# Kernel tuning notes

Hardware: AMD Instinct MI355X
Metric: run time of the kernel (lower is better)

Reference implementation:

```python
import jax, jax.numpy as jnp
import numpy as np

HEADS = 16
DIM_HEAD = 64
RMS_EPS = 1.1920929e-07  # torch.finfo(float32).eps (torch RMSNorm eps=None default)
ROPE_THETA = 10000.0


def _rope(x):
    # x: [b, h, n, d]; rotary-embedding-torch style interleaved rotation
    n, d = x.shape[-2], x.shape[-1]
    inv_freq = 1.0 / (ROPE_THETA ** (jnp.arange(0, d, 2, dtype=jnp.float32) / d))
    t = jnp.arange(n, dtype=jnp.float32)
    freqs = t[:, None] * inv_freq[None, :]              # [n, d/2]
    cos = jnp.repeat(jnp.cos(freqs), 2, axis=-1)        # [n, d] interleaved
    sin = jnp.repeat(jnp.sin(freqs), 2, axis=-1)
    x1 = x[..., ::2]
    x2 = x[..., 1::2]
    rot = jnp.stack((-x2, x1), axis=-1).reshape(x.shape)  # rotate_half, interleaved pairs
    return x * cos + rot * sin


def setup_inputs() -> dict:
    key = jax.random.key(0)
    ks = jax.random.split(key, 6)
    b, n, dim = 2, 2048, 1024
    tokens = jax.random.normal(ks[0], (b, n, dim), dtype=jnp.float32)
    norm_weight = jnp.ones((dim,), dtype=jnp.float32)
    wq = jax.random.normal(ks[1], (dim, dim), dtype=jnp.float32) * 0.02
    wk = jax.random.normal(ks[2], (dim, dim), dtype=jnp.float32) * 0.02
    wv = jax.random.normal(ks[3], (dim, dim), dtype=jnp.float32) * 0.02
    wo = jax.random.normal(ks[4], (dim, dim), dtype=jnp.float32) * 0.02
    return {"tokens": tokens, "norm_weight": norm_weight, "wq": wq, "wk": wk, "wv": wv, "wo": wo}


def reference(tokens, norm_weight, wq, wk, wv, wo):
    b, n, dim = tokens.shape
    # RMSNorm (elementwise affine)
    x = tokens * jax.lax.rsqrt(jnp.mean(tokens * tokens, axis=-1, keepdims=True) + RMS_EPS)
    x = x * norm_weight
    # QKV projections (torch Linear: x @ W.T), split heads: b n (h d) -> b h n d
    def split(y):
        return y.reshape(b, n, HEADS, DIM_HEAD).transpose(0, 2, 1, 3)
    q = split(x @ wq.T) * (DIM_HEAD ** -0.5)
    k = split(x @ wk.T)
    v = split(x @ wv.T)
    # rotary embedding (no kv cache -> same positions for q and k)
    q = _rope(q)
    k = _rope(k)
    sim = jnp.einsum('bhid,bhjd->bhij', q, k)
    causal = jnp.triu(jnp.ones((n, n), dtype=bool), k=1)
    sim = jnp.where(causal, -jnp.finfo(sim.dtype).max, sim)
    attn = jax.nn.softmax(sim, axis=-1)
    out = jnp.einsum('bhij,bhjd->bhid', attn, v)
    out = out.transpose(0, 2, 1, 3).reshape(b, n, dim)  # merge heads
    return out @ wo.T
```

## Files before the change

kernel.cpp:

```cpp
#include <hip/hip_runtime.h>

typedef __bf16 bf16x8 __attribute__((ext_vector_type(8)));
typedef float f32x4 __attribute__((ext_vector_type(4)));

#define DIM 1024
#define NSEQ 2048

#define GL2LDS(g, l) __builtin_amdgcn_global_load_lds( \
    (const __attribute__((address_space(1))) void*)(g), \
    (__attribute__((address_space(3))) void*)(l), 16, 0, 0)

#define MFMA16(a, b, c) __builtin_amdgcn_mfma_f32_16x16x32_bf16(a, b, c, 0, 0, 0)

__global__ __launch_bounds__(256) void cvt_kernel(const float* __restrict__ s,
                                                  __bf16* __restrict__ d) {
    int i = (blockIdx.x * 256 + threadIdx.x) * 4;
    float4 f = *(const float4*)(s + i);
    union { uint2 u; __bf16 h[4]; } p;
    p.h[0] = (__bf16)f.x; p.h[1] = (__bf16)f.y;
    p.h[2] = (__bf16)f.z; p.h[3] = (__bf16)f.w;
    *(uint2*)(d + i) = p.u;
}

__global__ __launch_bounds__(256) void pre_kernel(const float* __restrict__ wq,
                                                  const float* __restrict__ wk,
                                                  const float* __restrict__ wv,
                                                  __bf16* __restrict__ dq,
                                                  __bf16* __restrict__ dk,
                                                  __bf16* __restrict__ dv,
                                                  float2* __restrict__ tbl,
                                                  int* __restrict__ counters,
                                                  const float* __restrict__ x,
                                                  const float* __restrict__ g,
                                                  __bf16* __restrict__ xo) {
    int bid = blockIdx.x;
    int t = threadIdx.x;
    if (bid == 0 && t < 8) counters[t] = 0;
    if (bid < 3072) {
        int slice = bid >> 10;
        const float* s = slice == 0 ? wq : (slice == 1 ? wk : wv);
        __bf16*      d = slice == 0 ? dq : (slice == 1 ? dk : dv);
        int i = ((bid & 1023) * 256 + t) * 4;
        float4 f = *(const float4*)(s + i);
        union { uint2 u; __bf16 h[4]; } p;
        p.h[0] = (__bf16)f.x; p.h[1] = (__bf16)f.y;
        p.h[2] = (__bf16)f.z; p.h[3] = (__bf16)f.w;
        *(uint2*)(d + i) = p.u;
    } else if (bid < 3328) {
        int e = (bid - 3072) * 256 + t;
        int pos = e >> 5, dp = e & 31;
        float inv = __expf(-(float)dp * (9.210340371976184f / 32.0f));
        float sn, cs;
        sincosf((float)pos * inv, &sn, &cs);
        tbl[e] = make_float2(cs, sn);
    } else {
        int row = bid - 3328;
        float4 xv = ((const float4*)(x + (size_t)row * DIM))[t];
        float ss = xv.x*xv.x + xv.y*xv.y + xv.z*xv.z + xv.w*xv.w;
        #pragma unroll
        for (int off = 32; off; off >>= 1) ss += __shfl_xor(ss, off, 64);
        __shared__ float red[4];
        if ((t & 63) == 0) red[t >> 6] = ss;
        __syncthreads();
        ss = red[0] + red[1] + red[2] + red[3];
        float r = rsqrtf(ss * (1.0f / 1024.0f) + 1.1920929e-07f);
        float4 gv = ((const float4*)g)[t];
        union { uint2 u; __bf16 h[4]; } p;
        p.h[0] = (__bf16)(xv.x * r * gv.x);
        p.h[1] = (__bf16)(xv.y * r * gv.y);
        p.h[2] = (__bf16)(xv.z * r * gv.z);
        p.h[3] = (__bf16)(xv.w * r * gv.w);
        *(uint2*)(xo + (size_t)row * DIM + t * 4) = p.u;
    }
}

template <typename CT, bool ROPE>
__device__ __forceinline__ void gemm_body(const __bf16* __restrict__ A,
                                          const __bf16* __restrict__ B,
                                          CT* __restrict__ C,
                                          int mb, int nb, int ldc, float scale,
                                          __bf16* As, __bf16* Bs,
                                          const float2* __restrict__ tbl) {
    int t = threadIdx.x;
    int w = t >> 6, l = t & 63;
    int wm = (w >> 1) * 64, wn = (w & 1) * 64;
    int lrow = l & 15, lq = l >> 4;
    int sw = lrow & 7;
    f32x4 acc[4][4] = {};

    int srow = w * 32 + (l >> 3);
    int sc8 = ((l & 7) ^ ((l >> 3) & 7)) * 8;
    const __bf16* gA = A + (size_t)(mb * 128 + srow) * 1024 + sc8;
    const __bf16* gB = B + (size_t)(nb * 128 + srow) * 1024 + sc8;
    __bf16* lA = As + (size_t)(w * 32) * 64;
    __bf16* lB = Bs + (size_t)(w * 32) * 64;

    for (int kt = 0; kt < 16; ++kt) {
        int k0 = kt * 64;
        #pragma unroll
        for (int c = 0; c < 4; ++c) {
            GL2LDS(gA + (size_t)c * 8 * 1024 + k0, lA + c * 8 * 64);
            GL2LDS(gB + (size_t)c * 8 * 1024 + k0, lB + c * 8 * 64);
        }
        __syncthreads();
        #pragma unroll
        for (int ch = 0; ch < 2; ++ch) {
            bf16x8 af[4], bfr[4];
            #pragma unroll
            for (int i = 0; i < 4; ++i)
                af[i] = *(const bf16x8*)&As[(wm + i * 16 + lrow) * 64 + ((ch * 4 + lq) ^ sw) * 8];
            #pragma unroll
            for (int i = 0; i < 4; ++i)
                bfr[i] = *(const bf16x8*)&Bs[(wn + i * 16 + lrow) * 64 + ((ch * 4 + lq) ^ sw) * 8];
            #pragma unroll
            for (int rt = 0; rt < 4; ++rt)
                #pragma unroll
                for (int ct = 0; ct < 4; ++ct)
                    acc[rt][ct] = MFMA16(af[rt], bfr[ct], acc[rt][ct]);
        }
        __syncthreads();
    }
    #pragma unroll
    for (int rt = 0; rt < 4; ++rt)
        #pragma unroll
        for (int ct = 0; ct < 4; ++ct) {
            int colg = nb * 128 + wn + ct * 16 + lrow;
            int dp = ((ct * 16 + lrow) & 63) >> 1;
            #pragma unroll
            for (int r = 0; r < 4; ++r) {
                int rowg = mb * 128 + wm + rt * 16 + lq * 4 + r;
                float v = acc[rt][ct][r] * scale;
                if constexpr (ROPE) {
                    float p = __shfl_xor(v, 1, 64);
                    float2 cs = tbl[((rowg & (NSEQ - 1)) << 5) + dp];
                    v = (lrow & 1) ? (v * cs.x + p * cs.y)
                                   : (v * cs.x - p * cs.y);
                }
                C[(size_t)rowg * ldc + colg] = (CT)v;
            }
        }
}

__global__ __launch_bounds__(256) void qkv_kernel(const __bf16* __restrict__ x,
                                                  const __bf16* __restrict__ wq,
                                                  const __bf16* __restrict__ wk,
                                                  const __bf16* __restrict__ wv,
                                                  __bf16* __restrict__ qb,
                                                  __bf16* __restrict__ kb,
                                                  __bf16* __restrict__ vtb,
                                                  const float2* __restrict__ tbl) {
    __shared__ __bf16 As[128 * 64];
    __shared__ __bf16 Bs[128 * 64];
    int bm = blockIdx.x, bn = blockIdx.y, z = blockIdx.z;
    if (z == 0)      gemm_body<__bf16, true >(x,  wq, qb,  bm, bn, 1024,
                                       0.125f * 1.44269504088896340736f, As, Bs, tbl);
    else if (z == 1) gemm_body<__bf16, true >(x,  wk, kb,  bm, bn, 1024, 1.0f, As, Bs, tbl);
    else             gemm_body<__bf16, false>(wv, x,  vtb, bn, bm, 4096, 1.0f, As, Bs, tbl);
}

__global__ __launch_bounds__(256) void wo_kernel(const __bf16* __restrict__ A,
                                                 const __bf16* __restrict__ B,
                                                 float* __restrict__ C) {
    __shared__ __bf16 As[128 * 64];
    __shared__ __bf16 Bs[64 * 64];
    int mb = blockIdx.x, nb = blockIdx.y;
    int t = threadIdx.x;
    int w = t >> 6, l = t & 63;
    int wm = (w >> 1) * 64, wn = (w & 1) * 32;
    int lrow = l & 15, lq = l >> 4;
    int sw = lrow & 7;
    f32x4 acc[4][2] = {};

    int srowA = w * 32 + (l >> 3);
    int srowB = w * 16 + (l >> 3);
    int sc8 = ((l & 7) ^ ((l >> 3) & 7)) * 8;
    const __bf16* gA = A + (size_t)(mb * 128 + srowA) * 1024 + sc8;
    const __bf16* gB = B + (size_t)(nb * 64 + srowB) * 1024 + sc8;
    __bf16* lA = As + (size_t)(w * 32) * 64;
    __bf16* lB = Bs + (size_t)(w * 16) * 64;

    for (int kt = 0; kt < 16; ++kt) {
        int k0 = kt * 64;
        #pragma unroll
        for (int c = 0; c < 4; ++c)
            GL2LDS(gA + (size_t)c * 8 * 1024 + k0, lA + c * 8 * 64);
        #pragma unroll
        for (int c = 0; c < 2; ++c)
            GL2LDS(gB + (size_t)c * 8 * 1024 + k0, lB + c * 8 * 64);
        __syncthreads();
        #pragma unroll
        for (int ch = 0; ch < 2; ++ch) {
            bf16x8 af[4], bfr[2];
            #pragma unroll
            for (int i = 0; i < 4; ++i)
                af[i] = *(const bf16x8*)&As[(wm + i * 16 + lrow) * 64 + ((ch * 4 + lq) ^ sw) * 8];
            #pragma unroll
            for (int i = 0; i < 2; ++i)
                bfr[i] = *(const bf16x8*)&Bs[(wn + i * 16 + lrow) * 64 + ((ch * 4 + lq) ^ sw) * 8];
            #pragma unroll
            for (int rt = 0; rt < 4; ++rt)
                #pragma unroll
                for (int ct = 0; ct < 2; ++ct)
                    acc[rt][ct] = MFMA16(af[rt], bfr[ct], acc[rt][ct]);
        }
        __syncthreads();
    }
    #pragma unroll
    for (int rt = 0; rt < 4; ++rt)
        #pragma unroll
        for (int ct = 0; ct < 2; ++ct)
            #pragma unroll
            for (int r = 0; r < 4; ++r) {
                int row = mb * 128 + wm + rt * 16 + lq * 4 + r;
                int col = nb * 64 + wn + ct * 16 + lrow;
                C[(size_t)row * 1024 + col] = acc[rt][ct][r];
            }
}

__global__ __launch_bounds__(256, 3) void attn_kernel(const __bf16* __restrict__ q,
                                                      const __bf16* __restrict__ kk,
                                                      const __bf16* __restrict__ vt,
                                                      __bf16* __restrict__ o,
                                                      int* __restrict__ counters) {
    int xcd = blockIdx.x & 7;
    int t = threadIdx.x;
    int w = t >> 6, l = t & 63;
    int lrow = l & 15, lq = l >> 4;
    int rw = (w & 1) * 32;
    int par = w >> 1;
    int row0 = t >> 3;
    int cb = t & 7;

    __shared__ __bf16 Kt[2][64 * 64];
    __shared__ __bf16 Vs[2][64 * 64];
    __shared__ __bf16 Ps[4][32 * 72];
    __shared__ int s_item;
    __bf16* pw = Ps[w];

    for (;;) {
        if (t == 0) s_item = atomicAdd(&counters[xcd], 1);
        __syncthreads();
        int item = s_item;
        if (item >= 128) break;
        int iq = 31 - (item >> 2);
        int bh = xcd * 4 + (item & 3);
        int h = bh & 15;
        int b = bh >> 4;
        int rowbase = b * NSEQ;

        const __bf16* kbase = kk + (size_t)rowbase * DIM + h * 64;
        const __bf16* vbase = vt + (size_t)(h * 64) * 4096 + b * 2048;

        bf16x8 qf[2][2];
        #pragma unroll
        for (int g = 0; g < 2; ++g) {
            const __bf16* qp = q + (size_t)(rowbase + iq * 64 + rw + g * 16 + lrow) * DIM + h * 64;
            qf[g][0] = *(const bf16x8*)(qp + lq * 8);
            qf[g][1] = *(const bf16x8*)(qp + 32 + lq * 8);
        }

        f32x4 oacc[2][4] = {};
        float m_r[2] = {-1e30f, -1e30f};
        float l_r[2] = {0.0f, 0.0f};

        const __bf16* kg = kbase + (size_t)row0 * DIM + cb * 8;
        const __bf16* vg = vbase + (size_t)row0 * 4096 + cb * 8;
        int dsw0 = (row0 * 8 + (cb ^ (row0 & 7))) * 8;
        int dsw1 = ((row0 + 32) * 8 + (cb ^ (row0 & 7))) * 8;

        uint4 k0a, k0b, v0a, v0b, k1a, k1b, v1a, v1b;
        k0a = *(const uint4*)(kg);
        k0b = *(const uint4*)(kg + (size_t)32 * DIM);
        v0a = *(const uint4*)(vg);
        v0b = *(const uint4*)(vg + (size_t)32 * 4096);
        if (iq >= 1) {
            k1a = *(const uint4*)(kg + (size_t)64 * DIM);
            k1b = *(const uint4*)(kg + (size_t)96 * DIM);
            v1a = *(const uint4*)(vg + 64);
            v1b = *(const uint4*)(vg + (size_t)32 * 4096 + 64);
        }
        *(uint4*)&Kt[0][dsw0] = k0a; *(uint4*)&Kt[0][dsw1] = k0b;
        *(uint4*)&Vs[0][dsw0] = v0a; *(uint4*)&Vs[0][dsw1] = v0b;
        if (iq >= 1) {
            *(uint4*)&Kt[1][dsw0] = k1a; *(uint4*)&Kt[1][dsw1] = k1b;
            *(uint4*)&Vs[1][dsw0] = v1a; *(uint4*)&Vs[1][dsw1] = v1b;
        }
        __syncthreads();

        int R = (iq + 2) >> 1;
        for (int rd = 0; rd < R; ++rd) {
            int jt = 2 * rd + par;
            bool pf = (rd + 1 < R);
            if (pf) {
                int je = 2 * rd + 2;
                size_t ko = (size_t)je * 64 * DIM;
                k0a = *(const uint4*)(kg + ko);
                k0b = *(const uint4*)(kg + ko + (size_t)32 * DIM);
                v0a = *(const uint4*)(vg + je * 64);
                v0b = *(const uint4*)(vg + (size_t)32 * 4096 + je * 64);
                if (je + 1 <= iq) {
                    k1a = *(const uint4*)(kg + ko + (size_t)64 * DIM);
                    k1b = *(const uint4*)(kg + ko + (size_t)96 * DIM);
                    v1a = *(const uint4*)(vg + je * 64 + 64);
                    v1b = *(const uint4*)(vg + (size_t)32 * 4096 + je * 64 + 64);
                }
            }
            if (jt <= iq) {
                const __bf16* Kb = Kt[par];
                const __bf16* Vb = Vs[par];
                int sw = lrow & 7;
                f32x4 st[2][4];
                __builtin_amdgcn_s_setprio(1);
                #pragma unroll
                for (int ct = 0; ct < 4; ++ct) {
                    int rr = (ct * 16 + lrow) * 8;
                    bf16x8 ka0 = *(const bf16x8*)&Kb[(rr + (lq ^ sw)) * 8];
                    bf16x8 ka1 = *(const bf16x8*)&Kb[(rr + ((4 + lq) ^ sw)) * 8];
                    #pragma unroll
                    for (int g = 0; g < 2; ++g) {
                        f32x4 z = {};
                        z = MFMA16(ka0, qf[g][0], z);
                        z = MFMA16(ka1, qf[g][1], z);
                        st[g][ct] = z;
                    }
                }
                __builtin_amdgcn_s_setprio(0);
                if (jt == iq) {
                    #pragma unroll
                    for (int g = 0; g < 2; ++g) {
                        int qrel = rw + g * 16 + lrow;
                        #pragma unroll
                        for (int ct = 0; ct < 4; ++ct)
                            #pragma unroll
                            for (int r = 0; r < 4; ++r)
                                if (ct * 16 + lq * 4 + r > qrel) st[g][ct][r] = -3.0e38f;
                    }
                }
                #pragma unroll
                for (int g = 0; g < 2; ++g) {
                    float m0 = fmaxf(fmaxf(st[g][0][0], st[g][0][1]), fmaxf(st[g][0][2], st[g][0][3]));
                    float m1 = fmaxf(fmaxf(st[g][1][0], st[g][1][1]), fmaxf(st[g][1][2], st[g][1][3]));
                    float m2 = fmaxf(fmaxf(st[g][2][0], st[g][2][1]), fmaxf(st[g][2][2], st[g][2][3]));
                    float m3 = fmaxf(fmaxf(st[g][3][0], st[g][3][1]), fmaxf(st[g][3][2], st[g][3][3]));
                    float mx = fmaxf(fmaxf(m0, m1), fmaxf(m2, m3));
                    mx = fmaxf(mx, __shfl_xor(mx, 16, 64));
                    mx = fmaxf(mx, __shfl_xor(mx, 32, 64));
                    if (!__all(mx - m_r[g] <= 8.0f)) {
                        float mnew = fmaxf(m_r[g], mx);
                        float alpha = __builtin_amdgcn_exp2f(m_r[g] - mnew);
                        l_r[g] *= alpha;
                        #pragma unroll
                        for (int ct = 0; ct < 4; ++ct)
                            #pragma unroll
                            for (int r = 0; r < 4; ++r) oacc[g][ct][r] *= alpha;
                        m_r[g] = mnew;
                    }
                    float ps = 0.0f;
                    #pragma unroll
                    for (int ct = 0; ct < 4; ++ct)
                        #pragma unroll
                        for (int r = 0; r < 4; ++r) {
                            float p = __builtin_amdgcn_exp2f(st[g][ct][r] - m_r[g]);
                            st[g][ct][r] = p;
                            ps += p;
                        }
                    ps += __shfl_xor(ps, 16, 64);
                    ps += __shfl_xor(ps, 32, 64);
                    l_r[g] += ps;
                }
                #pragma unroll
                for (int g = 0; g < 2; ++g)
                    #pragma unroll
                    for (int ct = 0; ct < 4; ++ct) {
                        union { uint2 u; __bf16 h4[4]; } pk;
                        #pragma unroll
                        for (int r = 0; r < 4; ++r) pk.h4[r] = (__bf16)st[g][ct][r];
                        *(uint2*)&pw[(g * 16 + lrow) * 72 + ct * 16 + lq * 4] = pk.u;
                    }
                bf16x8 pb[2][2];
                #pragma unroll
                for (int g = 0; g < 2; ++g) {
                    pb[g][0] = *(const bf16x8*)&pw[(g * 16 + lrow) * 72 + lq * 8];
                    pb[g][1] = *(const bf16x8*)&pw[(g * 16 + lrow) * 72 + 32 + lq * 8];
                }
                __builtin_amdgcn_s_setprio(1);
                #pragma unroll
                for (int ct = 0; ct < 4; ++ct) {
                    int rr = (ct * 16 + lrow) * 8;
                    bf16x8 va0 = *(const bf16x8*)&Vb[(rr + (lq ^ sw)) * 8];
                    bf16x8 va1 = *(const bf16x8*)&Vb[(rr + ((4 + lq) ^ sw)) * 8];
                    #pragma unroll
                    for (int g = 0; g < 2; ++g) {
                        oacc[g][ct] = MFMA16(va0, pb[g][0], oacc[g][ct]);
                        oacc[g][ct] = MFMA16(va1, pb[g][1], oacc[g][ct]);
                    }
                }
                __builtin_amdgcn_s_setprio(0);
            }
            if (pf) {
                __syncthreads();
                *(uint4*)&Kt[0][dsw0] = k0a; *(uint4*)&Kt[0][dsw1] = k0b;
                *(uint4*)&Vs[0][dsw0] = v0a; *(uint4*)&Vs[0][dsw1] = v0b;
                if (2 * rd + 3 <= iq) {
                    *(uint4*)&Kt[1][dsw0] = k1a; *(uint4*)&Kt[1][dsw1] = k1b;
                    *(uint4*)&Vs[1][dsw0] = v1a; *(uint4*)&Vs[1][dsw1] = v1b;
                }
                __syncthreads();
            }
        }

        __syncthreads();
        float* sc = (float*)&Ps[0][0];
        float* base = sc + (w & 1) * 2304 + l * 36;
        if (par == 1) {
            #pragma unroll
            for (int g = 0; g < 2; ++g)
                #pragma unroll
                for (int ct = 0; ct < 4; ++ct)
                    *(f32x4*)(base + g * 16 + ct * 4) = oacc[g][ct];
            base[32] = m_r[0]; base[33] = m_r[1];
            base[34] = l_r[0]; base[35] = l_r[1];
        }
        __syncthreads();
        if (par == 0) {
            #pragma unroll
            for (int g = 0; g < 2; ++g) {
                float mb = base[32 + g], lb = base[34 + g];
                float m = fmaxf(m_r[g], mb);
                float a  = __builtin_amdgcn_exp2f(m_r[g] - m);
                float bb = __builtin_amdgcn_exp2f(mb - m);
                float rcp = 1.0f / (a * l_r[g] + bb * lb);
                const size_t orow = (size_t)(rowbase + iq * 64 + rw + g * 16 + lrow) * DIM + h * 64;
                #pragma unroll
                for (int ct = 0; ct < 4; ++ct) {
                    f32x4 ob = *(const f32x4*)(base + g * 16 + ct * 4);
                    union { uint2 u; __bf16 h4[4]; } pk;
                    #pragma unroll
                    for (int r = 0; r < 4; ++r)
                        pk.h4[r] = (__bf16)((a * oacc[g][ct][r] + bb * ob[r]) * rcp);
                    *(uint2*)(o + orow + ct * 16 + lq * 4) = pk.u;
                }
            }
        }
    }
}

extern "C" void kernel_launch(void* const* d_in, const int* in_sizes, int n_in,
                              void* d_out, int out_size, void* d_ws, size_t ws_size,
                              hipStream_t stream) {
    const float* tokens = (const float*)d_in[0];
    const float* gamma  = (const float*)d_in[1];
    const float* wq = (const float*)d_in[2];
    const float* wk = (const float*)d_in[3];
    const float* wv = (const float*)d_in[4];
    const float* wo = (const float*)d_in[5];

    __bf16* ws  = (__bf16*)d_ws;
    __bf16* x   = ws;
    __bf16* qb  = x   + (size_t)4096 * 1024;
    __bf16* kb  = qb  + (size_t)4096 * 1024;
    __bf16* vtb = kb  + (size_t)4096 * 1024;
    __bf16* ao  = x;
    __bf16* wob = qb;
    float*  out = (float*)d_out;

    __bf16* wqb = (__bf16*)d_out;
    __bf16* wkb = wqb + (size_t)1024 * 1024;
    __bf16* wvb = wkb + (size_t)1024 * 1024;
    float2* tbl = (float2*)((char*)d_out + (size_t)6 * 1024 * 1024);
    int* counters = (int*)((char*)d_out + (size_t)8 * 1024 * 1024);

    pre_kernel<<<7424, 256, 0, stream>>>(wq, wk, wv, wqb, wkb, wvb, tbl, counters,
                                         tokens, gamma, x);

    qkv_kernel<<<dim3(32, 8, 3), 256, 0, stream>>>(x, wqb, wkb, wvb, qb, kb, vtb, tbl);

    attn_kernel<<<768, 256, 0, stream>>>(qb, kb, vtb, ao, counters);

    cvt_kernel<<<1024, 256, 0, stream>>>(wo, wob);

    wo_kernel<<<dim3(32, 16), 256, 0, stream>>>(ao, wob, out);
}
```

Measured before the change: 193.9 us.

## Fuse Wo fp32-to-bf16 conversion into output GEMM and prefetch next attention item

```diff
diff --git a/kernel.cpp b/kernel.cpp
--- a/kernel.cpp
+++ b/kernel.cpp
@@ -11,16 +11,6 @@
     (__attribute__((address_space(3))) void*)(l), 16, 0, 0)
 
 #define MFMA16(a, b, c) __builtin_amdgcn_mfma_f32_16x16x32_bf16(a, b, c, 0, 0, 0)
-
-__global__ __launch_bounds__(256) void cvt_kernel(const float* __restrict__ s,
-                                                  __bf16* __restrict__ d) {
-    int i = (blockIdx.x * 256 + threadIdx.x) * 4;
-    float4 f = *(const float4*)(s + i);
-    union { uint2 u; __bf16 h[4]; } p;
-    p.h[0] = (__bf16)f.x; p.h[1] = (__bf16)f.y;
-    p.h[2] = (__bf16)f.z; p.h[3] = (__bf16)f.w;
-    *(uint2*)(d + i) = p.u;
-}
 
 __global__ __launch_bounds__(256) void pre_kernel(const float* __restrict__ wq,
                                                   const float* __restrict__ wk,
@@ -159,7 +149,7 @@
 }
 
 __global__ __launch_bounds__(256) void wo_kernel(const __bf16* __restrict__ A,
-                                                 const __bf16* __restrict__ B,
+                                                 const float* __restrict__ B,
                                                  float* __restrict__ C) {
     __shared__ __bf16 As[128 * 64];
     __shared__ __bf16 Bs[64 * 64];
@@ -172,21 +162,35 @@
     f32x4 acc[4][2] = {};
 
     int srowA = w * 32 + (l >> 3);
-    int srowB = w * 16 + (l >> 3);
     int sc8 = ((l & 7) ^ ((l >> 3) & 7)) * 8;
     const __bf16* gA = A + (size_t)(mb * 128 + srowA) * 1024 + sc8;
-    const __bf16* gB = B + (size_t)(nb * 64 + srowB) * 1024 + sc8;
     __bf16* lA = As + (size_t)(w * 32) * 64;
-    __bf16* lB = Bs + (size_t)(w * 16) * 64;
+
+    int rB = t >> 2;
+    const float* gB = B + (size_t)(nb * 64 + rB) * 1024 + (t & 3) * 16;
+    int db0 = (rB * 8 + (((t & 3) * 2    ) ^ (rB & 7))) * 8;
+    int db1 = (rB * 8 + (((t & 3) * 2 + 1) ^ (rB & 7))) * 8;
 
     for (int kt = 0; kt < 16; ++kt) {
         int k0 = kt * 64;
         #pragma unroll
         for (int c = 0; c < 4; ++c)
             GL2LDS(gA + (size_t)c * 8 * 1024 + k0, lA + c * 8 * 64);
-        #pragma unroll
-        for (int c = 0; c < 2; ++c)
-            GL2LDS(gB + (size_t)c * 8 * 1024 + k0, lB + c * 8 * 64);
+        float4 b0 = *(const float4*)(gB + k0);
+        float4 b1 = *(const float4*)(gB + k0 + 4);
+        float4 b2 = *(const float4*)(gB + k0 + 8);
+        float4 b3 = *(const float4*)(gB + k0 + 12);
+        union { uint4 u; __bf16 h[8]; } p0, p1;
+        p0.h[0] = (__bf16)b0.x; p0.h[1] = (__bf16)b0.y;
+        p0.h[2] = (__bf16)b0.z; p0.h[3] = (__bf16)b0.w;
+        p0.h[4] = (__bf16)b1.x; p0.h[5] = (__bf16)b1.y;
+        p0.h[6] = (__bf16)b1.z; p0.h[7] = (__bf16)b1.w;
+        p1.h[0] = (__bf16)b2.x; p1.h[1] = (__bf16)b2.y;
+        p1.h[2] = (__bf16)b2.z; p1.h[3] = (__bf16)b2.w;
+        p1.h[4] = (__bf16)b3.x; p1.h[5] = (__bf16)b3.y;
+        p1.h[6] = (__bf16)b3.z; p1.h[7] = (__bf16)b3.w;
+        *(uint4*)&Bs[db0] = p0.u;
+        *(uint4*)&Bs[db1] = p1.u;
         __syncthreads();
         #pragma unroll
         for (int ch = 0; ch < 2; ++ch) {
@@ -237,11 +241,16 @@
     __shared__ int s_item;
     __bf16* pw = Ps[w];
 
-    for (;;) {
-        if (t == 0) s_item = atomicAdd(&counters[xcd], 1);
-        __syncthreads();
-        int item = s_item;
-        if (item >= 128) break;
+    int dsw0 = (row0 * 8 + (cb ^ (row0 & 7))) * 8;
+    int dsw1 = ((row0 + 32) * 8 + (cb ^ (row0 & 7))) * 8;
+
+    if (t == 0) s_item = atomicAdd(&counters[xcd], 1);
+    __syncthreads();
+    int item = s_item;
+    bool pf_valid = false;
+    uint4 k0a, k0b, v0a, v0b, k1a, k1b, v1a, v1b;
+
+    while (item < 128) {
         int iq = 31 - (item >> 2);
         int bh = xcd * 4 + (item & 3);
         int h = bh & 15;
@@ -250,6 +259,8 @@
 
         const __bf16* kbase = kk + (size_t)rowbase * DIM + h * 64;
         const __bf16* vbase = vt + (size_t)(h * 64) * 4096 + b * 2048;
+        const __bf16* kg = kbase + (size_t)row0 * DIM + cb * 8;
+        const __bf16* vg = vbase + (size_t)row0 * 4096 + cb * 8;
 
         bf16x8 qf[2][2];
         #pragma unroll
@@ -263,21 +274,17 @@
         float m_r[2] = {-1e30f, -1e30f};
         float l_r[2] = {0.0f, 0.0f};
 
-        const __bf16* kg = kbase + (size_t)row0 * DIM + cb * 8;
-        const __bf16* vg = vbase + (size_t)row0 * 4096 + cb * 8;
-        int dsw0 = (row0 * 8 + (cb ^ (row0 & 7))) * 8;
-        int dsw1 = ((row0 + 32) * 8 + (cb ^ (row0 & 7))) * 8;
-
-        uint4 k0a, k0b, v0a, v0b, k1a, k1b, v1a, v1b;
-        k0a = *(const uint4*)(kg);
-        k0b = *(const uint4*)(kg + (size_t)32 * DIM);
-        v0a = *(const uint4*)(vg);
-        v0b = *(const uint4*)(vg + (size_t)32 * 4096);
-        if (iq >= 1) {
-            k1a = *(const uint4*)(kg + (size_t)64 * DIM);
-            k1b = *(const uint4*)(kg + (size_t)96 * DIM);
-            v1a = *(const uint4*)(vg + 64);
-            v1b = *(const uint4*)(vg + (size_t)32 * 4096 + 64);
+        if (!pf_valid) {
+            k0a = *(const uint4*)(kg);
+            k0b = *(const uint4*)(kg + (size_t)32 * DIM);
+            v0a = *(const uint4*)(vg);
+            v0b = *(const uint4*)(vg + (size_t)32 * 4096);
+            if (iq >= 1) {
+                k1a = *(const uint4*)(kg + (size_t)64 * DIM);
+                k1b = *(const uint4*)(kg + (size_t)96 * DIM);
+                v1a = *(const uint4*)(vg + 64);
+                v1b = *(const uint4*)(vg + (size_t)32 * 4096 + 64);
+            }
         }
         *(uint4*)&Kt[0][dsw0] = k0a; *(uint4*)&Kt[0][dsw1] = k0b;
         *(uint4*)&Vs[0][dsw0] = v0a; *(uint4*)&Vs[0][dsw1] = v0b;
@@ -289,6 +296,8 @@
 
         int R = (iq + 2) >> 1;
         for (int rd = 0; rd < R; ++rd) {
+            if (rd == R - 1 && t == 0)
+                s_item = atomicAdd(&counters[xcd], 1);
             int jt = 2 * rd + par;
             bool pf = (rd + 1 < R);
             if (pf) {
@@ -410,6 +419,25 @@
         }
 
         __syncthreads();
+        int nitem = s_item;
+        if (nitem < 128) {
+            int niq = 31 - (nitem >> 2);
+            int nbh = xcd * 4 + (nitem & 3);
+            int nh = nbh & 15;
+            int nb_ = nbh >> 4;
+            const __bf16* nkg = kk + ((size_t)(nb_ * NSEQ) + row0) * DIM + nh * 64 + cb * 8;
+            const __bf16* nvg = vt + (size_t)(nh * 64 + row0) * 4096 + nb_ * 2048 + cb * 8;
+            k0a = *(const uint4*)(nkg);
+            k0b = *(const uint4*)(nkg + (size_t)32 * DIM);
+            v0a = *(const uint4*)(nvg);
+            v0b = *(const uint4*)(nvg + (size_t)32 * 4096);
+            if (niq >= 1) {
+                k1a = *(const uint4*)(nkg + (size_t)64 * DIM);
+                k1b = *(const uint4*)(nkg + (size_t)96 * DIM);
+                v1a = *(const uint4*)(nvg + 64);
+                v1b = *(const uint4*)(nvg + (size_t)32 * 4096 + 64);
+            }
+        }
         float* sc = (float*)&Ps[0][0];
         float* base = sc + (w & 1) * 2304 + l * 36;
         if (par == 1) {
@@ -442,6 +470,8 @@
                 }
             }
         }
+        item = nitem;
+        pf_valid = true;
     }
 }
 
@@ -461,7 +491,6 @@
     __bf16* kb  = qb  + (size_t)4096 * 1024;
     __bf16* vtb = kb  + (size_t)4096 * 1024;
     __bf16* ao  = x;
-    __bf16* wob = qb;
     float*  out = (float*)d_out;
 
     __bf16* wqb = (__bf16*)d_out;
@@ -477,7 +506,5 @@
 
     attn_kernel<<<768, 256, 0, stream>>>(qb, kb, vtb, ao, counters);
 
-    cvt_kernel<<<1024, 256, 0, stream>>>(wo, wob);
-
-    wo_kernel<<<dim3(32, 16), 256, 0, stream>>>(ao, wob, out);
+    wo_kernel<<<dim3(32, 16), 256, 0, stream>>>(ao, wo, out);
 }
```

Measured after the change: 202.0 us (median of 2 runs). 1.04x slower.
